# Performance work log

Hardware: AMD Instinct MI355X
Metric: run time of the kernel (lower is better)

## Reference

```python
import jax, jax.numpy as jnp
import numpy as np

N = 10000
E = 320000
F_IN = 256
F_PROJ = 200


def setup_inputs() -> dict:
    key = jax.random.key(0)
    ks = jax.random.split(key, 8)
    x = jax.random.normal(ks[0], (N, F_IN), dtype=jnp.float32)
    edge_attr = jax.random.uniform(ks[1], (N, N), dtype=jnp.float32)
    src = jax.random.randint(ks[2], (E,), 0, N)
    dst = jax.random.randint(ks[3], (E,), 0, N)
    # remove self loops at data-gen time (module calls remove_self_loops)
    dst = jnp.where(dst == src, (dst + 1) % N, dst)
    edge_index = jnp.stack([src, dst]).astype(jnp.int64)
    W_proj = jax.random.normal(ks[4], (F_IN, F_PROJ), dtype=jnp.float32) * 0.05
    b_proj = jnp.zeros((F_PROJ,), dtype=jnp.float32)
    W_att = jax.random.normal(ks[5], (F_PROJ, 1), dtype=jnp.float32) * 0.05
    b_att = jnp.zeros((1,), dtype=jnp.float32)
    return {"x": x, "edge_attr": edge_attr, "edge_index": edge_index,
            "W_proj": W_proj, "b_proj": b_proj, "W_att": W_att, "b_att": b_att}


def reference(x, edge_attr, edge_index, W_proj, b_proj, W_att, b_att):
    src, dst = edge_index[0], edge_index[1]
    # gather: x_j = source features, x_i = target features (PyG default flow)
    x_i = x[dst]                      # [E, F_IN]
    x_j = x[src]                      # [E, F_IN]
    p_i = x_i @ W_proj + b_proj       # [E, 200]
    p_j = x_j @ W_proj + b_proj       # [E, 200]
    alpha = jnp.abs(p_i - p_j) @ W_att + b_att   # [E, 1]
    alpha = jax.nn.relu(alpha)
    alpha = jax.nn.softmax(alpha, axis=0)        # softmax over edges
    a = alpha[:, 0]
    # write attention symmetrically into the dense edge matrix
    edge_values = edge_attr.at[src, dst].set(a).at[dst, src].set(a)
    # scatter-max aggregation of (unprojected) x_i by target index
    agg = jax.ops.segment_max(x_i, dst, num_segments=N)
    agg = jnp.where(jnp.isfinite(agg), agg, jnp.zeros((), agg.dtype))
    return agg, edge_values
```

## Files before the change

### kernel.cpp

```cpp
#include <hip/hip_runtime.h>

#define N_NODES 10000
#define E_EDGES 320000
#define F_IN    256
#define F_PROJ  200

typedef float vfloat4 __attribute__((ext_vector_type(4)));

#define N4_TOTAL 25000000L
#define S1_SPLIT 4000000L

#define K1_PROJ_BLOCKS 1250
#define K1_COPY_BLOCKS 768
#define A_BLOCKS    2048
#define A_CHUNK     40
#define AGG_BLOCKS  160
#define AGG_N4      (N_NODES * F_IN / 4)
#define AGG_PER_BLK (AGG_N4 / AGG_BLOCKS)
#define K3_BLOCKS   4096

#define WS_P      0L
#define WS_EXP    4000000L
#define WS_FLAGS  5280000L
#define WS_SUM    5320000L

__device__ __forceinline__ unsigned short f32_to_bf16(float f) {
    unsigned int u = __float_as_uint(f);
    u += 0x7FFFu + ((u >> 16) & 1u);
    return (unsigned short)(u >> 16);
}
__device__ __forceinline__ float bf16_to_f32(unsigned short b) {
    return __uint_as_float(((unsigned int)b) << 16);
}

__global__ __launch_bounds__(256) void k1_proj_flags_copy(
        const float* __restrict__ x, const float* __restrict__ W,
        unsigned short* __restrict__ P, const int* __restrict__ ei,
        int* __restrict__ flags,
        const vfloat4* __restrict__ csrc, vfloat4* __restrict__ cdst) {
    int bid = blockIdx.x, tid = threadIdx.x;
    if (bid >= K1_PROJ_BLOCKS) {
        long i = (long)(bid - K1_PROJ_BLOCKS) * 256 + tid;
        const long stride = (long)K1_COPY_BLOCKS * 256;
        for (; i < S1_SPLIT; i += stride) {
            vfloat4 v = __builtin_nontemporal_load(csrc + i);
            __builtin_nontemporal_store(v, cdst + i);
        }
        return;
    }
    int gt = bid * 256 + tid;
    flags[ei[E_EDGES + gt]] = 1;

    __shared__ float xs[8][F_IN];
    int n0 = bid * 8;
    for (int i = tid; i < 8 * F_IN / 4; i += 256)
        ((float4*)xs)[i] = ((const float4*)(x + (long)n0 * F_IN))[i];
    __syncthreads();
    int j = tid;
    if (j >= F_PROJ) return;
    float acc[8] = {0.f,0.f,0.f,0.f,0.f,0.f,0.f,0.f};
    for (int k = 0; k < F_IN; ++k) {
        float w = W[k * F_PROJ + j];
        #pragma unroll
        for (int r = 0; r < 8; ++r) acc[r] += xs[r][k] * w;
    }
    #pragma unroll
    for (int r = 0; r < 8; ++r) P[(long)(n0 + r) * F_PROJ + j] = f32_to_bf16(acc[r]);
}

__global__ __launch_bounds__(256) void k2_alpha_agg(
        const int* __restrict__ ei, const unsigned short* __restrict__ P,
        const float* __restrict__ Watt, const float* __restrict__ batt,
        float* __restrict__ expalpha, float* __restrict__ sumbuf,
        const int* __restrict__ flags, const float4* __restrict__ x4,
        float4* __restrict__ agg4) {
    int bid = blockIdx.x, tid = threadIdx.x;
    if (bid < A_BLOCKS) {
        __shared__ float bsum;
        if (tid == 0) bsum = 0.f;
        __syncthreads();
        int wid  = bid * 4 + (tid >> 6);
        int lane = tid & 63;
        float4 w4 = make_float4(0.f, 0.f, 0.f, 0.f);
        if (lane < 50) w4 = ((const float4*)Watt)[lane];
        float bias = batt[0];
        int e0 = wid * A_CHUNK;
        int e1 = min(e0 + A_CHUNK, E_EDGES);
        float lsum = 0.f;
        for (int e = e0; e < e1; ++e) {
            int s = ei[e];
            int d = ei[E_EDGES + e];
            float acc = 0.f;
            if (lane < 50) {
                uint2 us = *(const uint2*)(P + (long)s * F_PROJ + lane * 4);
                uint2 ud = *(const uint2*)(P + (long)d * F_PROJ + lane * 4);
                acc = fabsf(bf16_to_f32((unsigned short)(ud.x & 0xFFFF)) -
                            bf16_to_f32((unsigned short)(us.x & 0xFFFF))) * w4.x
                    + fabsf(bf16_to_f32((unsigned short)(ud.x >> 16)) -
                            bf16_to_f32((unsigned short)(us.x >> 16))) * w4.y
                    + fabsf(bf16_to_f32((unsigned short)(ud.y & 0xFFFF)) -
                            bf16_to_f32((unsigned short)(us.y & 0xFFFF))) * w4.z
                    + fabsf(bf16_to_f32((unsigned short)(ud.y >> 16)) -
                            bf16_to_f32((unsigned short)(us.y >> 16))) * w4.w;
            }
            #pragma unroll
            for (int off = 32; off; off >>= 1) acc += __shfl_down(acc, off);
            if (lane == 0) {
                float ea = expf(fmaxf(acc + bias, 0.f));
                expalpha[e] = ea;
                lsum += ea;
            }
        }
        if (lane == 0) atomicAdd(&bsum, lsum);
        __syncthreads();
        if (tid == 0) atomicAdd(sumbuf, bsum);
        return;
    }
    long base = (long)(bid - A_BLOCKS) * AGG_PER_BLK;
    for (int i = tid; i < AGG_PER_BLK; i += 256) {
        long i4 = base + i;
        float4 v = x4[i4];
        if (!flags[i4 >> 6]) v = make_float4(0.f, 0.f, 0.f, 0.f);
        agg4[i4] = v;
    }
}

__global__ __launch_bounds__(256) void k3_copy(
        const vfloat4* __restrict__ src, vfloat4* __restrict__ dst) {
    long i = S1_SPLIT + (long)blockIdx.x * 256 + threadIdx.x;
    const long stride = (long)K3_BLOCKS * 256;
    for (; i + stride < N4_TOTAL; i += 2 * stride) {
        vfloat4 a = src[i];
        vfloat4 b = src[i + stride];
        dst[i] = a;
        dst[i + stride] = b;
    }
    if (i < N4_TOTAL) dst[i] = src[i];
}

__global__ __launch_bounds__(256) void k4_scatter(
        const int* __restrict__ ei, const float* __restrict__ expalpha,
        const float* __restrict__ sumbuf, float* __restrict__ ev) {
    int e = blockIdx.x * 256 + threadIdx.x;
    if (e >= E_EDGES) return;
    float a = expalpha[e] / sumbuf[0];
    int s = ei[e], d = ei[E_EDGES + e];
    ev[(long)s * N_NODES + d] = a;
    ev[(long)d * N_NODES + s] = a;
}

extern "C" void kernel_launch(void* const* d_in, const int* in_sizes, int n_in,
                              void* d_out, int out_size, void* d_ws, size_t ws_size,
                              hipStream_t stream) {
    (void)in_sizes; (void)n_in; (void)out_size; (void)ws_size;
    const float* x         = (const float*)d_in[0];
    const float* edge_attr = (const float*)d_in[1];
    const int*   ei        = (const int*)d_in[2];
    const float* W_proj    = (const float*)d_in[3];
    const float* W_att     = (const float*)d_in[5];
    const float* b_att     = (const float*)d_in[6];

    float* agg = (float*)d_out;
    float* ev  = (float*)d_out + (long)N_NODES * F_IN;
    char* ws = (char*)d_ws;

    unsigned short* P = (unsigned short*)(ws + WS_P);
    float* expalpha   = (float*)(ws + WS_EXP);
    int*   flags      = (int*)(ws + WS_FLAGS);
    float* sumbuf     = (float*)(ws + WS_SUM);

    hipMemsetAsync(ws + WS_FLAGS, 0, 40016, stream);

    k1_proj_flags_copy<<<K1_PROJ_BLOCKS + K1_COPY_BLOCKS, 256, 0, stream>>>(
        x, W_proj, P, ei, flags, (const vfloat4*)edge_attr, (vfloat4*)ev);

    k2_alpha_agg<<<A_BLOCKS + AGG_BLOCKS, 256, 0, stream>>>(
        ei, P, W_att, b_att, expalpha, sumbuf, flags,
        (const float4*)x, (float4*)agg);

    k3_copy<<<K3_BLOCKS, 256, 0, stream>>>(
        (const vfloat4*)edge_attr, (vfloat4*)ev);

    k4_scatter<<<(E_EDGES + 255) / 256, 256, 0, stream>>>(
        ei, expalpha, sumbuf, ev);
}
```

Before: 294.6 us.

## Replace custom edge_attr copy kernels with hipMemcpyAsync and shrink projection tiles

Removes the 400 MB copy that was split between the k1 side blocks and a separate k3 copy kernel, and does it with a single hipMemcpyAsync device-to-device before the compute kernels. The projection kernel now uses 4 nodes per block over 2500 blocks instead of 8 nodes over 1250, and a bounds check is added on the flag write. This gives up the overlap of copy with projection in exchange for the runtime's copy path and one fewer kernel launch, and it lowers weight reuse per block in the projection.

```diff
diff --git a/kernel.cpp b/kernel.cpp
--- a/kernel.cpp
+++ b/kernel.cpp
@@ -5,19 +5,14 @@
 #define F_IN    256
 #define F_PROJ  200
 
-typedef float vfloat4 __attribute__((ext_vector_type(4)));
+#define EV_BYTES 400000000L
 
-#define N4_TOTAL 25000000L
-#define S1_SPLIT 4000000L
-
-#define K1_PROJ_BLOCKS 1250
-#define K1_COPY_BLOCKS 768
-#define A_BLOCKS    2048
-#define A_CHUNK     40
-#define AGG_BLOCKS  160
-#define AGG_N4      (N_NODES * F_IN / 4)
+#define PJ_BLOCKS 2500
+#define A_BLOCKS  2048
+#define A_CHUNK   40
+#define AGG_BLOCKS 160
+#define AGG_N4    (N_NODES * F_IN / 4)
 #define AGG_PER_BLK (AGG_N4 / AGG_BLOCKS)
-#define K3_BLOCKS   4096
 
 #define WS_P      0L
 #define WS_EXP    4000000L
@@ -33,39 +28,28 @@
     return __uint_as_float(((unsigned int)b) << 16);
 }
 
-__global__ __launch_bounds__(256) void k1_proj_flags_copy(
+__global__ __launch_bounds__(256) void k1_proj_flags(
         const float* __restrict__ x, const float* __restrict__ W,
         unsigned short* __restrict__ P, const int* __restrict__ ei,
-        int* __restrict__ flags,
-        const vfloat4* __restrict__ csrc, vfloat4* __restrict__ cdst) {
+        int* __restrict__ flags) {
     int bid = blockIdx.x, tid = threadIdx.x;
-    if (bid >= K1_PROJ_BLOCKS) {
-        long i = (long)(bid - K1_PROJ_BLOCKS) * 256 + tid;
-        const long stride = (long)K1_COPY_BLOCKS * 256;
-        for (; i < S1_SPLIT; i += stride) {
-            vfloat4 v = __builtin_nontemporal_load(csrc + i);
-            __builtin_nontemporal_store(v, cdst + i);
-        }
-        return;
-    }
     int gt = bid * 256 + tid;
-    flags[ei[E_EDGES + gt]] = 1;
+    if (gt < E_EDGES) flags[ei[E_EDGES + gt]] = 1;
 
-    __shared__ float xs[8][F_IN];
-    int n0 = bid * 8;
-    for (int i = tid; i < 8 * F_IN / 4; i += 256)
-        ((float4*)xs)[i] = ((const float4*)(x + (long)n0 * F_IN))[i];
+    __shared__ float xs[4][F_IN];
+    int n0 = bid * 4;
+    ((float4*)xs)[tid] = ((const float4*)(x + (long)n0 * F_IN))[tid];
     __syncthreads();
     int j = tid;
     if (j >= F_PROJ) return;
-    float acc[8] = {0.f,0.f,0.f,0.f,0.f,0.f,0.f,0.f};
+    float acc[4] = {0.f, 0.f, 0.f, 0.f};
     for (int k = 0; k < F_IN; ++k) {
         float w = W[k * F_PROJ + j];
         #pragma unroll
-        for (int r = 0; r < 8; ++r) acc[r] += xs[r][k] * w;
+        for (int r = 0; r < 4; ++r) acc[r] += xs[r][k] * w;
     }
     #pragma unroll
-    for (int r = 0; r < 8; ++r) P[(long)(n0 + r) * F_PROJ + j] = f32_to_bf16(acc[r]);
+    for (int r = 0; r < 4; ++r) P[(long)(n0 + r) * F_PROJ + j] = f32_to_bf16(acc[r]);
 }
 
 __global__ __launch_bounds__(256) void k2_alpha_agg(
@@ -125,20 +109,7 @@
     }
 }
 
-__global__ __launch_bounds__(256) void k3_copy(
-        const vfloat4* __restrict__ src, vfloat4* __restrict__ dst) {
-    long i = S1_SPLIT + (long)blockIdx.x * 256 + threadIdx.x;
-    const long stride = (long)K3_BLOCKS * 256;
-    for (; i + stride < N4_TOTAL; i += 2 * stride) {
-        vfloat4 a = src[i];
-        vfloat4 b = src[i + stride];
-        dst[i] = a;
-        dst[i + stride] = b;
-    }
-    if (i < N4_TOTAL) dst[i] = src[i];
-}
-
-__global__ __launch_bounds__(256) void k4_scatter(
+__global__ __launch_bounds__(256) void k3_scatter(
         const int* __restrict__ ei, const float* __restrict__ expalpha,
         const float* __restrict__ sumbuf, float* __restrict__ ev) {
     int e = blockIdx.x * 256 + threadIdx.x;
@@ -171,16 +142,14 @@
 
     hipMemsetAsync(ws + WS_FLAGS, 0, 40016, stream);
 
-    k1_proj_flags_copy<<<K1_PROJ_BLOCKS + K1_COPY_BLOCKS, 256, 0, stream>>>(
-        x, W_proj, P, ei, flags, (const vfloat4*)edge_attr, (vfloat4*)ev);
+    hipMemcpyAsync(ev, edge_attr, EV_BYTES, hipMemcpyDeviceToDevice, stream);
+
+    k1_proj_flags<<<PJ_BLOCKS, 256, 0, stream>>>(x, W_proj, P, ei, flags);
 
     k2_alpha_agg<<<A_BLOCKS + AGG_BLOCKS, 256, 0, stream>>>(
         ei, P, W_att, b_att, expalpha, sumbuf, flags,
         (const float4*)x, (float4*)agg);
 
-    k3_copy<<<K3_BLOCKS, 256, 0, stream>>>(
-        (const vfloat4*)edge_attr, (vfloat4*)ev);
-
-    k4_scatter<<<(E_EDGES + 255) / 256, 256, 0, stream>>>(
+    k3_scatter<<<(E_EDGES + 255) / 256, 256, 0, stream>>>(
         ei, expalpha, sumbuf, ev);
 }
```

Measured after the change: 296.3 us. About the same (+0.6%).

## Fuse remaining edge_attr copy into alpha kernel with interleaved block roles

Applied to the files above, without the earlier changes.

Merges the separate bulk copy kernel into the alpha/aggregation kernel. Every fourth block computes alpha and then its share of agg, and the other three blocks stream the rest of the dense matrix with wider 4x nontemporal loads and stores. The latency-bound gather work is meant to overlap the bandwidth-bound copy, and one launch goes away. The risk is interference between the two kinds of blocks and a larger per-wave edge chunk for alpha.

```diff
diff --git a/kernel.cpp b/kernel.cpp
--- a/kernel.cpp
+++ b/kernel.cpp
@@ -12,12 +12,13 @@
 
 #define K1_PROJ_BLOCKS 1250
 #define K1_COPY_BLOCKS 768
-#define A_BLOCKS    2048
-#define A_CHUNK     40
-#define AGG_BLOCKS  160
-#define AGG_N4      (N_NODES * F_IN / 4)
-#define AGG_PER_BLK (AGG_N4 / AGG_BLOCKS)
-#define K3_BLOCKS   4096
+#define K2_BLOCKS 6144
+#define K2_ALPHA_BLOCKS 1536
+#define K2_COPY_BLOCKS (K2_BLOCKS - K2_ALPHA_BLOCKS)
+#define K2_ALPHA_WAVES (K2_ALPHA_BLOCKS * 4)
+#define ALPHA_CHUNK ((E_EDGES + K2_ALPHA_WAVES - 1) / K2_ALPHA_WAVES)
+#define AGG_N4 (N_NODES * F_IN / 4)
+#define AGG_CHUNK ((AGG_N4 + K2_ALPHA_BLOCKS - 1) / K2_ALPHA_BLOCKS)
 
 #define WS_P      0L
 #define WS_EXP    4000000L
@@ -33,6 +34,23 @@
     return __uint_as_float(((unsigned int)b) << 16);
 }
 
+__device__ __forceinline__ void nt_copy_wide(
+        const vfloat4* __restrict__ src, vfloat4* __restrict__ dst,
+        long beg, long end, long cid, long nblk, int tid) {
+    long i = beg + (cid * 256 + tid) * 4;
+    const long stride = nblk * 256 * 4;
+    for (; i < end; i += stride) {
+        vfloat4 v0 = __builtin_nontemporal_load(src + i);
+        vfloat4 v1 = __builtin_nontemporal_load(src + i + 1);
+        vfloat4 v2 = __builtin_nontemporal_load(src + i + 2);
+        vfloat4 v3 = __builtin_nontemporal_load(src + i + 3);
+        __builtin_nontemporal_store(v0, dst + i);
+        __builtin_nontemporal_store(v1, dst + i + 1);
+        __builtin_nontemporal_store(v2, dst + i + 2);
+        __builtin_nontemporal_store(v3, dst + i + 3);
+    }
+}
+
 __global__ __launch_bounds__(256) void k1_proj_flags_copy(
         const float* __restrict__ x, const float* __restrict__ W,
         unsigned short* __restrict__ P, const int* __restrict__ ei,
@@ -40,12 +58,8 @@
         const vfloat4* __restrict__ csrc, vfloat4* __restrict__ cdst) {
     int bid = blockIdx.x, tid = threadIdx.x;
     if (bid >= K1_PROJ_BLOCKS) {
-        long i = (long)(bid - K1_PROJ_BLOCKS) * 256 + tid;
-        const long stride = (long)K1_COPY_BLOCKS * 256;
-        for (; i < S1_SPLIT; i += stride) {
-            vfloat4 v = __builtin_nontemporal_load(csrc + i);
-            __builtin_nontemporal_store(v, cdst + i);
-        }
+        nt_copy_wide(csrc, cdst, 0L, S1_SPLIT,
+                     bid - K1_PROJ_BLOCKS, K1_COPY_BLOCKS, tid);
         return;
     }
     int gt = bid * 256 + tid;
@@ -68,77 +82,65 @@
     for (int r = 0; r < 8; ++r) P[(long)(n0 + r) * F_PROJ + j] = f32_to_bf16(acc[r]);
 }
 
-__global__ __launch_bounds__(256) void k2_alpha_agg(
+__global__ __launch_bounds__(256) void k2_alpha_agg_copy(
         const int* __restrict__ ei, const unsigned short* __restrict__ P,
         const float* __restrict__ Watt, const float* __restrict__ batt,
         float* __restrict__ expalpha, float* __restrict__ sumbuf,
         const int* __restrict__ flags, const float4* __restrict__ x4,
-        float4* __restrict__ agg4) {
+        float4* __restrict__ agg4,
+        const vfloat4* __restrict__ csrc, vfloat4* __restrict__ cdst) {
     int bid = blockIdx.x, tid = threadIdx.x;
-    if (bid < A_BLOCKS) {
-        __shared__ float bsum;
-        if (tid == 0) bsum = 0.f;
-        __syncthreads();
-        int wid  = bid * 4 + (tid >> 6);
-        int lane = tid & 63;
-        float4 w4 = make_float4(0.f, 0.f, 0.f, 0.f);
-        if (lane < 50) w4 = ((const float4*)Watt)[lane];
-        float bias = batt[0];
-        int e0 = wid * A_CHUNK;
-        int e1 = min(e0 + A_CHUNK, E_EDGES);
-        float lsum = 0.f;
-        for (int e = e0; e < e1; ++e) {
-            int s = ei[e];
-            int d = ei[E_EDGES + e];
-            float acc = 0.f;
-            if (lane < 50) {
-                uint2 us = *(const uint2*)(P + (long)s * F_PROJ + lane * 4);
-                uint2 ud = *(const uint2*)(P + (long)d * F_PROJ + lane * 4);
-                acc = fabsf(bf16_to_f32((unsigned short)(ud.x & 0xFFFF)) -
-                            bf16_to_f32((unsigned short)(us.x & 0xFFFF))) * w4.x
-                    + fabsf(bf16_to_f32((unsigned short)(ud.x >> 16)) -
-                            bf16_to_f32((unsigned short)(us.x >> 16))) * w4.y
-                    + fabsf(bf16_to_f32((unsigned short)(ud.y & 0xFFFF)) -
-                            bf16_to_f32((unsigned short)(us.y & 0xFFFF))) * w4.z
-                    + fabsf(bf16_to_f32((unsigned short)(ud.y >> 16)) -
-                            bf16_to_f32((unsigned short)(us.y >> 16))) * w4.w;
-            }
-            #pragma unroll
-            for (int off = 32; off; off >>= 1) acc += __shfl_down(acc, off);
-            if (lane == 0) {
-                float ea = expf(fmaxf(acc + bias, 0.f));
-                expalpha[e] = ea;
-                lsum += ea;
-            }
-        }
-        if (lane == 0) atomicAdd(&bsum, lsum);
-        __syncthreads();
-        if (tid == 0) atomicAdd(sumbuf, bsum);
+    int role = bid & 3;
+    if (role != 0) {
+        long cid = (long)(bid >> 2) * 3 + (role - 1);
+        nt_copy_wide(csrc, cdst, S1_SPLIT, N4_TOTAL, cid, K2_COPY_BLOCKS, tid);
         return;
     }
-    long base = (long)(bid - A_BLOCKS) * AGG_PER_BLK;
-    for (int i = tid; i < AGG_PER_BLK; i += 256) {
-        long i4 = base + i;
-        float4 v = x4[i4];
-        if (!flags[i4 >> 6]) v = make_float4(0.f, 0.f, 0.f, 0.f);
-        agg4[i4] = v;
+    __shared__ float bsum;
+    if (tid == 0) bsum = 0.f;
+    __syncthreads();
+    int aid = bid >> 2, wid = aid * 4 + (tid >> 6), lane = tid & 63;
+    float4 w4 = make_float4(0.f, 0.f, 0.f, 0.f);
+    if (lane < 50) w4 = ((const float4*)Watt)[lane];
+    float bias = batt[0];
+    int e0 = wid * ALPHA_CHUNK, e1 = min(e0 + ALPHA_CHUNK, E_EDGES);
+    float lsum = 0.f;
+    for (int e = e0; e < e1; ++e) {
+        int s = ei[e], d = ei[E_EDGES + e];
+        float acc = 0.f;
+        if (lane < 50) {
+            uint2 us = *(const uint2*)(P + (long)s * F_PROJ + lane * 4);
+            uint2 ud = *(const uint2*)(P + (long)d * F_PROJ + lane * 4);
+            acc = fabsf(bf16_to_f32((unsigned short)(ud.x & 0xFFFF)) -
+                        bf16_to_f32((unsigned short)(us.x & 0xFFFF))) * w4.x
+                + fabsf(bf16_to_f32((unsigned short)(ud.x >> 16)) -
+                        bf16_to_f32((unsigned short)(us.x >> 16))) * w4.y
+                + fabsf(bf16_to_f32((unsigned short)(ud.y & 0xFFFF)) -
+                        bf16_to_f32((unsigned short)(us.y & 0xFFFF))) * w4.z
+                + fabsf(bf16_to_f32((unsigned short)(ud.y >> 16)) -
+                        bf16_to_f32((unsigned short)(us.y >> 16))) * w4.w;
+        }
+        #pragma unroll
+        for (int off = 32; off; off >>= 1) acc += __shfl_down(acc, off);
+        if (lane == 0) {
+            float ea = expf(fmaxf(acc + bias, 0.f));
+            expalpha[e] = ea;
+            lsum += ea;
+        }
+    }
+    if (lane == 0) atomicAdd(&bsum, lsum);
+    __syncthreads();
+    if (tid == 0) atomicAdd(sumbuf, bsum);
+    long a0 = (long)aid * AGG_CHUNK;
+    long a1 = a0 + AGG_CHUNK; if (a1 > AGG_N4) a1 = AGG_N4;
+    for (long i = a0 + tid; i < a1; i += 256) {
+        float4 v = x4[i];
+        if (!flags[i >> 6]) v = make_float4(0.f, 0.f, 0.f, 0.f);
+        agg4[i] = v;
     }
 }
 
-__global__ __launch_bounds__(256) void k3_copy(
-        const vfloat4* __restrict__ src, vfloat4* __restrict__ dst) {
-    long i = S1_SPLIT + (long)blockIdx.x * 256 + threadIdx.x;
-    const long stride = (long)K3_BLOCKS * 256;
-    for (; i + stride < N4_TOTAL; i += 2 * stride) {
-        vfloat4 a = src[i];
-        vfloat4 b = src[i + stride];
-        dst[i] = a;
-        dst[i + stride] = b;
-    }
-    if (i < N4_TOTAL) dst[i] = src[i];
-}
-
-__global__ __launch_bounds__(256) void k4_scatter(
+__global__ __launch_bounds__(256) void k3_scatter(
         const int* __restrict__ ei, const float* __restrict__ expalpha,
         const float* __restrict__ sumbuf, float* __restrict__ ev) {
     int e = blockIdx.x * 256 + threadIdx.x;
@@ -174,13 +176,11 @@
     k1_proj_flags_copy<<<K1_PROJ_BLOCKS + K1_COPY_BLOCKS, 256, 0, stream>>>(
         x, W_proj, P, ei, flags, (const vfloat4*)edge_attr, (vfloat4*)ev);
 
-    k2_alpha_agg<<<A_BLOCKS + AGG_BLOCKS, 256, 0, stream>>>(
+    k2_alpha_agg_copy<<<K2_BLOCKS, 256, 0, stream>>>(
         ei, P, W_att, b_att, expalpha, sumbuf, flags,
-        (const float4*)x, (float4*)agg);
-
-    k3_copy<<<K3_BLOCKS, 256, 0, stream>>>(
+        (const float4*)x, (float4*)agg,
         (const vfloat4*)edge_attr, (vfloat4*)ev);
 
-    k4_scatter<<<(E_EDGES + 255) / 256, 256, 0, stream>>>(
+    k3_scatter<<<(E_EDGES + 255) / 256, 256, 0, stream>>>(
         ei, expalpha, sumbuf, ev);
 }
```

Result: slower. 708.2 us (+140.4%).
